# Kernel optimization log

Measured on AMD Instinct MI355X. Metric: run time of the kernel, lower is better.

## Reference

```python
import jax, jax.numpy as jnp
import numpy as np

NEG_INF = -1e30  # stand-in for float('-inf') that is softmax-safe


def setup_inputs() -> dict:
    key = jax.random.key(0)
    ks = jax.random.split(key, 6)
    B, H, S, D = 2, 8, 1024, 64
    NF, K = 4, 3
    return {
        "query": jax.random.normal(ks[0], (B, H, S, D), dtype=jnp.float32),
        "keys": jax.random.normal(ks[1], (B, H, S, D), dtype=jnp.float32),
        "vals": jax.random.normal(ks[2], (B, H, S, D), dtype=jnp.float32),
        "mask": jnp.ones((B, 1, S, S), dtype=jnp.int32),
        "conv_w": jax.random.normal(ks[3], (NF, 1, K, K), dtype=jnp.float32) * (1.0 / K),
        "conv_b": jnp.zeros((NF,), dtype=jnp.float32),
        "lin_w": jax.random.normal(ks[4], (1, NF), dtype=jnp.float32) * 0.5,
        "lin_b": jnp.zeros((1,), dtype=jnp.float32),
    }


def reference(query, keys, vals, mask, conv_w, conv_b, lin_w, lin_b):
    B, H, S, D = query.shape
    NF = conv_w.shape[0]
    K = conv_w.shape[2]
    scale = jnp.asarray(D, query.dtype) ** 0.5

    # [B,H,S,S] raw dot-product scores
    dp = jnp.einsum("bhsd,bhtd->bhst", query, keys) / scale

    # conv2d over the score matrix: treat (B*H) as batch, 1 input channel
    x = dp.reshape(B * H, 1, S, S)
    conv = jax.lax.conv_general_dilated(
        x, conv_w,
        window_strides=(1, 1),
        padding=[(K // 2, K // 2), (K // 2, K // 2)],
        dimension_numbers=("NCHW", "OIHW", "NCHW"),
    ) + conv_b[None, :, None, None]
    conv = jax.nn.leaky_relu(conv, negative_slope=0.01)  # [B*H, NF, S, S]

    # per-pixel linear over the filter axis (Linear(num_filters, 1))
    conv = conv.reshape(B, H, NF, S, S)
    preattn = jnp.einsum("bhfst,f->bhst", conv, lin_w[0]) + lin_b[0]

    # masking + softmax (mask broadcasts over heads)
    preattn = jnp.where(mask == 0, jnp.asarray(NEG_INF, preattn.dtype), preattn)
    attn = jax.nn.softmax(preattn, axis=-1)

    # dropout is identity in eval mode
    return jnp.einsum("bhst,bhtd->bhsd", attn, vals)
```

## Files before the change

kernel.cpp:

```cpp
#include <hip/hip_runtime.h>
#include <math.h>

#define S_LEN 1024
#define D_DIM 64
#define NBH   16
#define RPB   14
#define NSB   74

typedef unsigned short ushort_t;
typedef unsigned int uint_t;
typedef __attribute__((ext_vector_type(8))) _Float16 half8;
typedef __attribute__((ext_vector_type(2))) _Float16 h2;
typedef __attribute__((ext_vector_type(4))) short short4v;
typedef __attribute__((ext_vector_type(4))) float f32x4;

__device__ __forceinline__ ushort_t f16bits(float x) {
    _Float16 h = (_Float16)x;
    ushort_t b;
    __builtin_memcpy(&b, &h, 2);
    return b;
}
__device__ __forceinline__ float uniform_f(float x) {
    return __int_as_float(__builtin_amdgcn_readfirstlane(__float_as_int(x)));
}
__device__ __forceinline__ float fast_exp2(float x) {
#if __has_builtin(__builtin_amdgcn_exp2f)
    return __builtin_amdgcn_exp2f(x);
#else
    return exp2f(x);
#endif
}
__device__ __forceinline__ half8 mk8(uint2 a, uint2 b) {
    union { uint_t u[4]; half8 h; } c;
    c.u[0] = a.x; c.u[1] = a.y; c.u[2] = b.x; c.u[3] = b.y;
    return c.h;
}
__device__ __forceinline__ int swz(int row, int unit) {
    return (row << 4) + (((unit + (row >> 2)) & 3) << 2);
}

__global__ __launch_bounds__(256) void prep(
    const float* __restrict__ k, const float* __restrict__ v,
    const int* __restrict__ mask, const float* __restrict__ conv_w,
    ushort_t* __restrict__ kh, ushort_t* __restrict__ vh,
    unsigned* __restrict__ mw, ushort_t* __restrict__ wtab)
{
    __shared__ float Ls[64][65];
    const int tid = threadIdx.x;
    const int bx = blockIdx.x;
    if (bx < 512) {
        const int gid  = bx * 256 + tid;
        const int bh   = gid >> 13;
        const int tile = (gid >> 7) & 63;
        const int ch   = (gid >> 6) & 1;
        const int lane = gid & 63;
        const int quad = lane >> 4, t15 = lane & 15;
        const float* src = k + ((size_t)bh * S_LEN + tile * 16 + t15) * D_DIM
                             + ch * 32 + quad * 8;
        float x[8];
        *(float4*)(x + 0) = *(const float4*)(src);
        *(float4*)(x + 4) = *(const float4*)(src + 4);
        ushort_t hv[8];
        #pragma unroll
        for (int i = 0; i < 8; ++i) hv[i] = f16bits(x[i] * 0.125f);
        *(short4v*)(kh + (size_t)gid * 8)     = *(short4v*)(hv);
        *(short4v*)(kh + (size_t)gid * 8 + 4) = *(short4v*)(hv + 4);
    } else if (bx < 768) {
        const int bi = bx - 512;
        const int tt = bi & 15, bh = bi >> 4;
        const float* vb = v + ((size_t)bh * S_LEN + tt * 64) * D_DIM;
        #pragma unroll
        for (int p = 0; p < 4; ++p) {
            int idx = p * 1024 + tid * 4;
            int r = idx >> 6, c = idx & 63;
            float4 x = *(const float4*)(vb + r * 64 + c);
            Ls[r][c] = x.x; Ls[r][c+1] = x.y; Ls[r][c+2] = x.z; Ls[r][c+3] = x.w;
        }
        __syncthreads();
        const int d = tid >> 2, c0 = (tid & 3) * 16;
        ushort_t hi[16];
        #pragma unroll
        for (int j = 0; j < 16; ++j) hi[j] = f16bits(Ls[c0 + j][d]);
        const int tb0 = tt * 8 + (c0 >> 3);
        const size_t o0 = (((size_t)bh * 128 + tb0) * 64 + d) * 8;
        const size_t o1 = (((size_t)bh * 128 + tb0 + 1) * 64 + d) * 8;
        *(short4v*)(vh + o0)     = *(short4v*)(hi);
        *(short4v*)(vh + o0 + 4) = *(short4v*)(hi + 4);
        *(short4v*)(vh + o1)     = *(short4v*)(hi + 8);
        *(short4v*)(vh + o1 + 4) = *(short4v*)(hi + 12);
    } else if (bx < 1024) {
        const int gid = (bx - 768) * 256 + tid;
        const int row = gid >> 5, wd = gid & 31;
        const int4* mp = (const int4*)(mask + (size_t)row * 1024 + wd * 32);
        unsigned bits = 0;
        #pragma unroll
        for (int p = 0; p < 8; ++p) {
            int4 qv = mp[p];
            bits |= (qv.x != 0 ? 1u : 0u) << (p * 4 + 0);
            bits |= (qv.y != 0 ? 1u : 0u) << (p * 4 + 1);
            bits |= (qv.z != 0 ? 1u : 0u) << (p * 4 + 2);
            bits |= (qv.w != 0 ? 1u : 0u) << (p * 4 + 3);
        }
        mw[(size_t)row * 32 + wd] = bits;
    } else {
        if (tid < 64) {
            const int o = tid & 15, qd = tid >> 4;
            half8* wt = (half8*)wtab;
            #pragma unroll
            for (int f = 0; f < 4; ++f) {
                half8 fr0 = {}, fr1 = {}, fr2 = {};
                #pragma unroll
                for (int i = 0; i < 8; ++i) {
                    const int kk = qd * 8 + i;
                    const int r  = kk & 15;
                    const bool hiK = kk < 16;
                    #pragma unroll
                    for (int dr = 0; dr < 3; ++dr) {
                        if (r - o == dr - 1) {
                            const float w0 = conv_w[f*9 + dr*3 + 0];
                            const float w1 = conv_w[f*9 + dr*3 + 1];
                            const float w2 = conv_w[f*9 + dr*3 + 2];
                            const _Float16 w0h = (_Float16)w0;
                            const _Float16 w1h = (_Float16)w1;
                            const _Float16 w2h = (_Float16)w2;
                            const _Float16 w0l = (_Float16)(w0 - (float)w0h);
                            const _Float16 w1l = (_Float16)(w1 - (float)w1h);
                            const _Float16 w2l = (_Float16)(w2 - (float)w2h);
                            fr0[i] = hiK ? w0h : w1h;
                            fr1[i] = hiK ? w0l : w1l;
                            fr2[i] = hiK ? w2h : w2l;
                        }
                    }
                }
                wt[(f*64 + tid)*3 + 0] = fr0;
                wt[(f*64 + tid)*3 + 1] = fr1;
                wt[(f*64 + tid)*3 + 2] = fr2;
            }
        }
    }
}

#define PSTR 1032
__global__ __launch_bounds__(512, 3) void fused_qk_conv_av(
    const float* __restrict__ q,
    const ushort_t* __restrict__ kh, const unsigned* __restrict__ mw,
    const ushort_t* __restrict__ vh, const ushort_t* __restrict__ wtab,
    const float* __restrict__ conv_b,
    const float* __restrict__ lin_w, const float* __restrict__ lin_b,
    float* __restrict__ out)
{
    __shared__ ushort_t sBuf[16512];
    __shared__ float oBuf[16][68];
    __shared__ float lsRow[16];
    __shared__ unsigned mbT[32][16];

    const int st = blockIdx.x, bh = blockIdx.y;
    const int s0 = st * RPB;
    const int b  = bh >> 3;
    const int tid = threadIdx.x;
    const int wave = tid >> 6, lane = tid & 63;
    const int m = lane & 15, quad = lane >> 4;

    {
        const int wd = tid >> 4, o = tid & 15;
        const int s = s0 - 1 + o;
        mbT[wd][o] = (s >= 0 && s < S_LEN)
                   ? mw[((size_t)b * S_LEN + s) * 32 + wd] : 0u;
    }
    if (wave == 0 && lane < 16) sBuf[(1    << 4) + lane] = 0;
    if (wave == 7 && lane < 16) sBuf[(1026 << 4) + lane] = 0;

    const int sA = s0 - 1 + m;
    const int sQ = sA < 0 ? 0 : (sA > S_LEN - 1 ? S_LEN - 1 : sA);
    const float* qp = q + ((size_t)bh * S_LEN + sQ) * D_DIM + quad * 8;
    float qa[16];
    *(float4*)(qa + 0)  = *(const float4*)(qp + 0);
    *(float4*)(qa + 4)  = *(const float4*)(qp + 4);
    *(float4*)(qa + 8)  = *(const float4*)(qp + 32);
    *(float4*)(qa + 12) = *(const float4*)(qp + 36);
    half8 AH0, AH1;
    #pragma unroll
    for (int i = 0; i < 8; ++i) {
        AH0[i] = (_Float16)qa[i];
        AH1[i] = (_Float16)qa[8 + i];
    }

    #pragma unroll
    for (int tt = 0; tt < 8; ++tt) {
        const int tile = wave * 8 + tt;
        const size_t kb = (((size_t)bh * 64 + tile) * 128 + lane) * 8;
        half8 KH0 = *(const half8*)(kh + kb);
        half8 KH1 = *(const half8*)(kh + kb + 512);
        f32x4 a = {0.f, 0.f, 0.f, 0.f};
        a = __builtin_amdgcn_mfma_f32_16x16x32_f16(AH0, KH0, a, 0, 0, 0);
        a = __builtin_amdgcn_mfma_f32_16x16x32_f16(AH1, KH1, a, 0, 0, 0);
        ushort_t t4[4];
        #pragma unroll
        for (int r = 0; r < 4; ++r) {
            const int s = s0 - 1 + quad * 4 + r;
            const float v = (s >= 0 && s < S_LEN) ? a[r] : 0.f;
            t4[r] = f16bits(v);
        }
        uint2 wv2;
        wv2.x = (uint_t)t4[0] | ((uint_t)t4[1] << 16);
        wv2.y = (uint_t)t4[2] | ((uint_t)t4[3] << 16);
        *(uint2*)&sBuf[swz(tile * 16 + m + 2, quad)] = wv2;
    }
    #pragma unroll
    for (int hsel = 0; hsel < 2; ++hsel) {
        const int tile = hsel ? (wave * 8 + 8) : (wave * 8 - 1);
        const int wantM = hsel ? 0 : 15;
        if (tile >= 0 && tile < 64) {
            const size_t kb = (((size_t)bh * 64 + tile) * 128 + lane) * 8;
            half8 KH0 = *(const half8*)(kh + kb);
            half8 KH1 = *(const half8*)(kh + kb + 512);
            f32x4 a = {0.f, 0.f, 0.f, 0.f};
            a = __builtin_amdgcn_mfma_f32_16x16x32_f16(AH0, KH0, a, 0, 0, 0);
            a = __builtin_amdgcn_mfma_f32_16x16x32_f16(AH1, KH1, a, 0, 0, 0);
            if (m == wantM) {
                ushort_t t4[4];
                #pragma unroll
                for (int r = 0; r < 4; ++r) {
                    const int s = s0 - 1 + quad * 4 + r;
                    const float v = (s >= 0 && s < S_LEN) ? a[r] : 0.f;
                    t4[r] = f16bits(v);
                }
                uint2 wv2;
                wv2.x = (uint_t)t4[0] | ((uint_t)t4[1] << 16);
                wv2.y = (uint_t)t4[2] | ((uint_t)t4[3] << 16);
                *(uint2*)&sBuf[swz(tile * 16 + m + 2, quad)] = wv2;
            }
        }
    }

    const float L2E = 1.44269504088896341f;
    const float lbE = uniform_f(lin_b[0] * L2E);


    const int u0 = (quad & 1) << 1;
    const int rB = m + 1 + (quad >> 1);
    uint_t Ps[16];
    #pragma unroll
    for (int p = 0; p < 4; ++p) {
        const int tileA = wave * 8 + p * 2;
        const int baseA = tileA * 16;
        half8 BA01 = mk8(*(const uint2*)&sBuf[swz(baseA + rB, u0)],
                         *(const uint2*)&sBuf[swz(baseA + rB, u0 + 1)]);
        half8 BA22 = mk8(*(const uint2*)&sBuf[swz(baseA + m + 3, u0)],
                         *(const uint2*)&sBuf[swz(baseA + m + 3, u0 + 1)]);
        half8 BB01 = mk8(*(const uint2*)&sBuf[swz(baseA + 16 + rB, u0)],
                         *(const uint2*)&sBuf[swz(baseA + 16 + rB, u0 + 1)]);
        half8 BB22 = mk8(*(const uint2*)&sBuf[swz(baseA + 16 + m + 3, u0)],
                         *(const uint2*)&sBuf[swz(baseA + 16 + m + 3, u0 + 1)]);
        float preA[4], preB[4];
        #pragma unroll
        for (int r = 0; r < 4; ++r) { preA[r] = lbE; preB[r] = lbE; }
        #pragma unroll 1
        for (int f = 0; f < 4; ++f) {
            const float cbf = uniform_f(conv_b[f]);
            const float lwf = lin_w[f];
            const float af  = uniform_f(0.505f * lwf * L2E);
            const float bf2 = uniform_f(0.495f * lwf * L2E);
            const half8* wp = (const half8*)wtab + (f * 64 + lane) * 3;
            const half8 W0 = wp[0];
            const half8 W1 = wp[1];
            const half8 W2 = wp[2];
            f32x4 aA = {0.f, 0.f, 0.f, 0.f};
            f32x4 aB = {0.f, 0.f, 0.f, 0.f};
            aA = __builtin_amdgcn_mfma_f32_16x16x32_f16(W0, BA01, aA, 0, 0, 0);
            aB = __builtin_amdgcn_mfma_f32_16x16x32_f16(W0, BB01, aB, 0, 0, 0);
            aA = __builtin_amdgcn_mfma_f32_16x16x32_f16(W1, BA01, aA, 0, 0, 0);
            aB = __builtin_amdgcn_mfma_f32_16x16x32_f16(W1, BB01, aB, 0, 0, 0);
            aA = __builtin_amdgcn_mfma_f32_16x16x32_f16(W2, BA22, aA, 0, 0, 0);
            aB = __builtin_amdgcn_mfma_f32_16x16x32_f16(W2, BB22, aB, 0, 0, 0);
            #pragma unroll
            for (int r = 0; r < 4; ++r) {
                const float yA = aA[r] + cbf, yB = aB[r] + cbf;
                preA[r] = fmaf(af, yA, preA[r]);
                preA[r] = fmaf(bf2, fabsf(yA), preA[r]);
                preB[r] = fmaf(af, yB, preB[r]);
                preB[r] = fmaf(bf2, fabsf(yB), preB[r]);
            }
        }
        const uint4 mq = *(const uint4*)&mbT[(tileA >> 1)][quad * 4];
        float pvA[4], pvB[4];
        #pragma unroll
        for (int r = 0; r < 4; ++r) {
            const int o = quad * 4 + r;
            const bool act = (o >= 1) && (o <= RPB) && (s0 - 1 + o < S_LEN);
            const unsigned mword = (r == 0) ? mq.x : (r == 1) ? mq.y
                                 : (r == 2) ? mq.z : mq.w;
            const bool kA = act && ((mword >> m) & 1u);
            const bool kB = act && ((mword >> (16 + m)) & 1u);
            pvA[r] = fast_exp2(kA ? preA[r] : -1e30f);
            pvB[r] = fast_exp2(kB ? preB[r] : -1e30f);
        }
        Ps[p*4 + 0] = (uint_t)f16bits(pvA[0]) | ((uint_t)f16bits(pvA[1]) << 16);
        Ps[p*4 + 1] = (uint_t)f16bits(pvA[2]) | ((uint_t)f16bits(pvA[3]) << 16);
        Ps[p*4 + 2] = (uint_t)f16bits(pvB[0]) | ((uint_t)f16bits(pvB[1]) << 16);
        Ps[p*4 + 3] = (uint_t)f16bits(pvB[2]) | ((uint_t)f16bits(pvB[3]) << 16);
    }
    __syncthreads();

    #pragma unroll
    for (int tt = 0; tt < 8; ++tt) {
        const int c = (wave * 8 + tt) * 16 + m;
        ushort_t* pp = &sBuf[quad * 4 * PSTR + c];
        const uint_t lo = Ps[2*tt], hi = Ps[2*tt + 1];
        pp[0]        = (ushort_t)lo;
        pp[PSTR]     = (ushort_t)(lo >> 16);
        pp[2*PSTR]   = (ushort_t)hi;
        pp[3*PSTR]   = (ushort_t)(hi >> 16);
    }
    __syncthreads();

    const int d0 = (wave & 3) * 16;
    const int th = wave >> 2;
    f32x4 O  = {0.f, 0.f, 0.f, 0.f};
    f32x4 RS = {0.f, 0.f, 0.f, 0.f};
    half8 ONE;
    #pragma unroll
    for (int i = 0; i < 8; ++i) ONE[i] = (_Float16)1.0f;
    const ushort_t* ph_base = &sBuf[m * PSTR + th * 512 + quad * 8];
    const ushort_t* vv_base = vh + ((size_t)bh * 65536
                                    + (size_t)(th * 64 + quad) * 512
                                    + (size_t)(d0 + m) * 8);
    #pragma unroll 4
    for (int i = 0; i < 16; ++i) {
        half8 ph = *(const half8*)(ph_base + i * 32);
        half8 vv = *(const half8*)(vv_base + (size_t)i * 2048);
        O  = __builtin_amdgcn_mfma_f32_16x16x32_f16(ph, vv, O, 0, 0, 0);
        RS = __builtin_amdgcn_mfma_f32_16x16x32_f16(ph, ONE, RS, 0, 0, 0);
    }
    if (wave < 4) {
        #pragma unroll
        for (int r = 0; r < 4; ++r) oBuf[quad * 4 + r][d0 + m] = O[r];
    }
    if (wave == 0 && m == 0) {
        #pragma unroll
        for (int r = 0; r < 4; ++r) lsRow[quad * 4 + r] = RS[r];
    }
    __syncthreads();
    if (wave >= 4) {
        #pragma unroll
        for (int r = 0; r < 4; ++r) {
            const int br = quad * 4 + r;
            const int s = s0 - 1 + br;
            if (br >= 1 && br <= RPB && s < S_LEN) {
                const float lsum = lsRow[br] + RS[r];
                out[((size_t)bh * S_LEN + s) * D_DIM + d0 + m] =
                    (O[r] + oBuf[br][d0 + m]) / lsum;
            }
        }
    }
}

extern "C" void kernel_launch(void* const* d_in, const int* in_sizes, int n_in,
                              void* d_out, int out_size, void* d_ws, size_t ws_size,
                              hipStream_t stream) {
    const float* q      = (const float*)d_in[0];
    const float* k      = (const float*)d_in[1];
    const float* v      = (const float*)d_in[2];
    const int*   mask   = (const int*)d_in[3];
    const float* conv_w = (const float*)d_in[4];
    const float* conv_b = (const float*)d_in[5];
    const float* lin_w  = (const float*)d_in[6];
    const float* lin_b  = (const float*)d_in[7];
    float* out = (float*)d_out;

    char* wsb = (char*)d_ws;
    const size_t MB = 1024 * 1024;
    ushort_t* kh   = (ushort_t*)(wsb + 0 * MB);
    ushort_t* vh   = (ushort_t*)(wsb + 2 * MB);
    unsigned* mw   = (unsigned*)(wsb + 4 * MB);
    ushort_t* wtab = (ushort_t*)(wsb + 4 * MB + 256 * 1024);

    prep<<<dim3(1025), 256, 0, stream>>>(k, v, mask, conv_w, kh, vh, mw, wtab);
    fused_qk_conv_av<<<dim3(NSB, NBH), 512, 0, stream>>>(
        q, kh, mw, vh, wtab, conv_b, lin_w, lin_b, out);
}
```

Before: 125.0 us.

## Keep softmax probabilities in registers and compute PV per-wave via bpermute

The conv MFMA operands are swapped so each wave's output tile is transposed, with rows along lanes. The probability tiles then stay in registers and are regathered with ds_bpermute into the PV MFMA operand layout. This removes the LDS round-trip for the P matrix and one block barrier. Each wave now computes a partial PV product over its own key range for all 64 output dims. The row sums come from a register reduction, and an LDS cross-wave reduction combines the partial outputs. The cost is more bpermute traffic, more V loads per wave, and an 8-way reduction over a 32KB buffer.

```diff
diff --git a/kernel.cpp b/kernel.cpp
--- a/kernel.cpp
+++ b/kernel.cpp
@@ -10,7 +10,6 @@
 typedef unsigned short ushort_t;
 typedef unsigned int uint_t;
 typedef __attribute__((ext_vector_type(8))) _Float16 half8;
-typedef __attribute__((ext_vector_type(2))) _Float16 h2;
 typedef __attribute__((ext_vector_type(4))) short short4v;
 typedef __attribute__((ext_vector_type(4))) float f32x4;
 
@@ -140,7 +139,6 @@
     }
 }
 
-#define PSTR 1032
 __global__ __launch_bounds__(512, 3) void fused_qk_conv_av(
     const float* __restrict__ q,
     const ushort_t* __restrict__ kh, const unsigned* __restrict__ mw,
@@ -149,10 +147,9 @@
     const float* __restrict__ lin_w, const float* __restrict__ lin_b,
     float* __restrict__ out)
 {
-    __shared__ ushort_t sBuf[16512];
-    __shared__ float oBuf[16][68];
-    __shared__ float lsRow[16];
+    __shared__ __align__(16) ushort_t sBuf[16512];
     __shared__ unsigned mbT[32][16];
+    __shared__ float rsP[8][16];
 
     const int st = blockIdx.x, bh = blockIdx.y;
     const int s0 = st * RPB;
@@ -236,25 +233,20 @@
     const float L2E = 1.44269504088896341f;
     const float lbE = uniform_f(lin_b[0] * L2E);
 
-
     const int u0 = (quad & 1) << 1;
     const int rB = m + 1 + (quad >> 1);
-    uint_t Ps[16];
-    #pragma unroll
-    for (int p = 0; p < 4; ++p) {
-        const int tileA = wave * 8 + p * 2;
-        const int baseA = tileA * 16;
-        half8 BA01 = mk8(*(const uint2*)&sBuf[swz(baseA + rB, u0)],
-                         *(const uint2*)&sBuf[swz(baseA + rB, u0 + 1)]);
-        half8 BA22 = mk8(*(const uint2*)&sBuf[swz(baseA + m + 3, u0)],
-                         *(const uint2*)&sBuf[swz(baseA + m + 3, u0 + 1)]);
-        half8 BB01 = mk8(*(const uint2*)&sBuf[swz(baseA + 16 + rB, u0)],
-                         *(const uint2*)&sBuf[swz(baseA + 16 + rB, u0 + 1)]);
-        half8 BB22 = mk8(*(const uint2*)&sBuf[swz(baseA + 16 + m + 3, u0)],
-                         *(const uint2*)&sBuf[swz(baseA + 16 + m + 3, u0 + 1)]);
-        float preA[4], preB[4];
-        #pragma unroll
-        for (int r = 0; r < 4; ++r) { preA[r] = lbE; preB[r] = lbE; }
+    const bool act = (m >= 1) && (m <= RPB) && (s0 - 1 + m < S_LEN);
+    uint_t PK[8][2];
+    float rs = 0.f;
+    #pragma unroll
+    for (int T = 0; T < 8; ++T) {
+        const int Tg = wave * 8 + T;
+        const int base = Tg * 16;
+        half8 A01 = mk8(*(const uint2*)&sBuf[swz(base + rB, u0)],
+                        *(const uint2*)&sBuf[swz(base + rB, u0 + 1)]);
+        half8 A22 = mk8(*(const uint2*)&sBuf[swz(base + m + 3, u0)],
+                        *(const uint2*)&sBuf[swz(base + m + 3, u0 + 1)]);
+        float pre[4] = {lbE, lbE, lbE, lbE};
         #pragma unroll 1
         for (int f = 0; f < 4; ++f) {
             const float cbf = uniform_f(conv_b[f]);
@@ -265,92 +257,91 @@
             const half8 W0 = wp[0];
             const half8 W1 = wp[1];
             const half8 W2 = wp[2];
-            f32x4 aA = {0.f, 0.f, 0.f, 0.f};
-            f32x4 aB = {0.f, 0.f, 0.f, 0.f};
-            aA = __builtin_amdgcn_mfma_f32_16x16x32_f16(W0, BA01, aA, 0, 0, 0);
-            aB = __builtin_amdgcn_mfma_f32_16x16x32_f16(W0, BB01, aB, 0, 0, 0);
-            aA = __builtin_amdgcn_mfma_f32_16x16x32_f16(W1, BA01, aA, 0, 0, 0);
-            aB = __builtin_amdgcn_mfma_f32_16x16x32_f16(W1, BB01, aB, 0, 0, 0);
-            aA = __builtin_amdgcn_mfma_f32_16x16x32_f16(W2, BA22, aA, 0, 0, 0);
-            aB = __builtin_amdgcn_mfma_f32_16x16x32_f16(W2, BB22, aB, 0, 0, 0);
+            f32x4 a = {0.f, 0.f, 0.f, 0.f};
+            a = __builtin_amdgcn_mfma_f32_16x16x32_f16(A01, W0, a, 0, 0, 0);
+            a = __builtin_amdgcn_mfma_f32_16x16x32_f16(A01, W1, a, 0, 0, 0);
+            a = __builtin_amdgcn_mfma_f32_16x16x32_f16(A22, W2, a, 0, 0, 0);
             #pragma unroll
             for (int r = 0; r < 4; ++r) {
-                const float yA = aA[r] + cbf, yB = aB[r] + cbf;
-                preA[r] = fmaf(af, yA, preA[r]);
-                preA[r] = fmaf(bf2, fabsf(yA), preA[r]);
-                preB[r] = fmaf(af, yB, preB[r]);
-                preB[r] = fmaf(bf2, fabsf(yB), preB[r]);
+                const float y = a[r] + cbf;
+                pre[r] = fmaf(af, y, pre[r]);
+                pre[r] = fmaf(bf2, fabsf(y), pre[r]);
             }
         }
-        const uint4 mq = *(const uint4*)&mbT[(tileA >> 1)][quad * 4];
-        float pvA[4], pvB[4];
+        const unsigned mword = mbT[Tg >> 1][m];
+        const int bb = ((Tg & 1) << 4) + quad * 4;
+        float pv[4];
         #pragma unroll
         for (int r = 0; r < 4; ++r) {
-            const int o = quad * 4 + r;
-            const bool act = (o >= 1) && (o <= RPB) && (s0 - 1 + o < S_LEN);
-            const unsigned mword = (r == 0) ? mq.x : (r == 1) ? mq.y
-                                 : (r == 2) ? mq.z : mq.w;
-            const bool kA = act && ((mword >> m) & 1u);
-            const bool kB = act && ((mword >> (16 + m)) & 1u);
-            pvA[r] = fast_exp2(kA ? preA[r] : -1e30f);
-            pvB[r] = fast_exp2(kB ? preB[r] : -1e30f);
-        }
-        Ps[p*4 + 0] = (uint_t)f16bits(pvA[0]) | ((uint_t)f16bits(pvA[1]) << 16);
-        Ps[p*4 + 1] = (uint_t)f16bits(pvA[2]) | ((uint_t)f16bits(pvA[3]) << 16);
-        Ps[p*4 + 2] = (uint_t)f16bits(pvB[0]) | ((uint_t)f16bits(pvB[1]) << 16);
-        Ps[p*4 + 3] = (uint_t)f16bits(pvB[2]) | ((uint_t)f16bits(pvB[3]) << 16);
-    }
+            const bool keep = act && ((mword >> (bb + r)) & 1u);
+            pv[r] = fast_exp2(keep ? pre[r] : -1e30f);
+            rs += pv[r];
+        }
+        PK[T][0] = (uint_t)f16bits(pv[0]) | ((uint_t)f16bits(pv[1]) << 16);
+        PK[T][1] = (uint_t)f16bits(pv[2]) | ((uint_t)f16bits(pv[3]) << 16);
+    }
+    rs += __shfl_xor(rs, 16);
+    rs += __shfl_xor(rs, 32);
+    if (quad == 0) rsP[wave][m] = rs;
+
+    f32x4 acc[4] = {{0,0,0,0},{0,0,0,0},{0,0,0,0},{0,0,0,0}};
+    const int addrA = (m + 32 * (quad & 1)) * 4;
+    const int addrB = addrA + 64;
+    const bool selHi = (quad & 2) != 0;
+    #pragma unroll
+    for (int kt = 0; kt < 4; ++kt) {
+        const int e0 = (int)PK[2*kt][0],     e1 = (int)PK[2*kt][1];
+        const int f0 = (int)PK[2*kt + 1][0], f1 = (int)PK[2*kt + 1][1];
+        const uint_t gA0 = (uint_t)__builtin_amdgcn_ds_bpermute(addrA, e0);
+        const uint_t gA1 = (uint_t)__builtin_amdgcn_ds_bpermute(addrA, e1);
+        const uint_t hA0 = (uint_t)__builtin_amdgcn_ds_bpermute(addrA, f0);
+        const uint_t hA1 = (uint_t)__builtin_amdgcn_ds_bpermute(addrA, f1);
+        const uint_t gB0 = (uint_t)__builtin_amdgcn_ds_bpermute(addrB, e0);
+        const uint_t gB1 = (uint_t)__builtin_amdgcn_ds_bpermute(addrB, e1);
+        const uint_t hB0 = (uint_t)__builtin_amdgcn_ds_bpermute(addrB, f0);
+        const uint_t hB1 = (uint_t)__builtin_amdgcn_ds_bpermute(addrB, f1);
+        union { uint_t u[4]; half8 h; } pf;
+        pf.u[0] = selHi ? hA0 : gA0;
+        pf.u[1] = selHi ? hA1 : gA1;
+        pf.u[2] = selHi ? hB0 : gB0;
+        pf.u[3] = selHi ? hB1 : gB1;
+        const size_t tb = (size_t)bh * 128 + wave * 16 + kt * 4 + quad;
+        #pragma unroll
+        for (int dt = 0; dt < 4; ++dt) {
+            half8 vv = *(const half8*)(vh + (tb * 64 + dt * 16 + m) * 8);
+            acc[dt] = __builtin_amdgcn_mfma_f32_16x16x32_f16(vv, pf.h, acc[dt], 0, 0, 0);
+        }
+    }
+
     __syncthreads();
 
-    #pragma unroll
-    for (int tt = 0; tt < 8; ++tt) {
-        const int c = (wave * 8 + tt) * 16 + m;
-        ushort_t* pp = &sBuf[quad * 4 * PSTR + c];
-        const uint_t lo = Ps[2*tt], hi = Ps[2*tt + 1];
-        pp[0]        = (ushort_t)lo;
-        pp[PSTR]     = (ushort_t)(lo >> 16);
-        pp[2*PSTR]   = (ushort_t)hi;
-        pp[3*PSTR]   = (ushort_t)(hi >> 16);
+    float* pbuf = (float*)sBuf;
+    #pragma unroll
+    for (int dt = 0; dt < 4; ++dt) {
+        #pragma unroll
+        for (int r = 0; r < 4; ++r) {
+            const int d = dt * 16 + quad * 4 + r;
+            pbuf[(wave * 16 + m) * 64 + (d ^ ((m & 7) << 2))] = acc[dt][r];
+        }
     }
     __syncthreads();
 
-    const int d0 = (wave & 3) * 16;
-    const int th = wave >> 2;
-    f32x4 O  = {0.f, 0.f, 0.f, 0.f};
-    f32x4 RS = {0.f, 0.f, 0.f, 0.f};
-    half8 ONE;
-    #pragma unroll
-    for (int i = 0; i < 8; ++i) ONE[i] = (_Float16)1.0f;
-    const ushort_t* ph_base = &sBuf[m * PSTR + th * 512 + quad * 8];
-    const ushort_t* vv_base = vh + ((size_t)bh * 65536
-                                    + (size_t)(th * 64 + quad) * 512
-                                    + (size_t)(d0 + m) * 8);
-    #pragma unroll 4
-    for (int i = 0; i < 16; ++i) {
-        half8 ph = *(const half8*)(ph_base + i * 32);
-        half8 vv = *(const half8*)(vv_base + (size_t)i * 2048);
-        O  = __builtin_amdgcn_mfma_f32_16x16x32_f16(ph, vv, O, 0, 0, 0);
-        RS = __builtin_amdgcn_mfma_f32_16x16x32_f16(ph, ONE, RS, 0, 0, 0);
-    }
-    if (wave < 4) {
-        #pragma unroll
-        for (int r = 0; r < 4; ++r) oBuf[quad * 4 + r][d0 + m] = O[r];
-    }
-    if (wave == 0 && m == 0) {
-        #pragma unroll
-        for (int r = 0; r < 4; ++r) lsRow[quad * 4 + r] = RS[r];
-    }
-    __syncthreads();
-    if (wave >= 4) {
-        #pragma unroll
-        for (int r = 0; r < 4; ++r) {
-            const int br = quad * 4 + r;
-            const int s = s0 - 1 + br;
-            if (br >= 1 && br <= RPB && s < S_LEN) {
-                const float lsum = lsRow[br] + RS[r];
-                out[((size_t)bh * S_LEN + s) * D_DIM + d0 + m] =
-                    (O[r] + oBuf[br][d0 + m]) / lsum;
+    #pragma unroll
+    for (int e = 0; e < 2; ++e) {
+        const int id = tid + e * 512;
+        if (id < 896) {
+            const int o = (id >> 6) + 1;
+            const int d = id & 63;
+            const int dx = d ^ ((o & 7) << 2);
+            float sum = 0.f, ls = 0.f;
+            #pragma unroll
+            for (int w = 0; w < 8; ++w) {
+                sum += pbuf[(w * 16 + o) * 64 + dx];
+                ls  += rsP[w][o];
             }
+            const int s = s0 - 1 + o;
+            if (s < S_LEN)
+                out[((size_t)bh * S_LEN + s) * D_DIM + d] = sum / ls;
         }
     }
 }
```

Result: slower. 132.6 us (+6.1%).
